# Performance work log

Hardware: AMD Instinct MI355X
Metric: run time of the kernel (lower is better)

The kernel has to match this reference:

```python
import jax, jax.numpy as jnp
import numpy as np

B, T, D, H = 2, 2048, 1024, 16
HD = D // H


def sinusoidal_rel_pe(seq_len, d_model, dtype=jnp.float32):
    # Relative positions T-1 .. 0 (reversed), standard sin/cos interleave.
    pos = jnp.arange(seq_len - 1, -1, -1, dtype=jnp.float32)[:, None]  # [T,1]
    div = jnp.exp(-jnp.log(jnp.float32(10000.0)) * jnp.arange(0, d_model, 2, dtype=jnp.float32) / d_model)
    pe = jnp.zeros((seq_len, d_model), dtype=jnp.float32)
    pe = pe.at[:, 0::2].set(jnp.sin(pos * div))
    pe = pe.at[:, 1::2].set(jnp.cos(pos * div))
    return pe.astype(dtype)


def relative_to_absolute(x):
    # x: [B,H,T,L] with L == T. Music-Transformer skew trick.
    b, h, t1, l = x.shape
    x = jnp.pad(x, ((0, 0), (0, 0), (0, 0), (1, 0)))          # pad left of last dim
    x = x.reshape(b, h, -1)
    x = jnp.pad(x, ((0, 0), (0, 0), (l - t1, 0)))
    x = x.reshape(b, h, 1 + t1, l)
    return x[:, :, 1:]


def setup_inputs() -> dict:
    key = jax.random.key(0)
    k1, k2, k3 = jax.random.split(key, 3)
    x = jax.random.normal(k1, (B, T, D), dtype=jnp.float32)
    # causal mask: True where attention is disallowed (j > i)
    mask = jnp.triu(jnp.ones((T, T), dtype=bool), k=1)[None, None]
    mask = jnp.broadcast_to(mask, (B, 1, T, T))
    Wqkv = jax.random.normal(k2, (D, 3 * D), dtype=jnp.float32) * 0.02
    Wout = jax.random.normal(k3, (D, D), dtype=jnp.float32) * 0.02
    bout = jnp.zeros((D,), dtype=jnp.float32)
    return {"x": x, "mask": mask, "Wqkv": Wqkv, "Wout": Wout, "bout": bout}


def reference(x, mask, Wqkv, Wout, bout):
    b, t, d = x.shape
    scale = jnp.sqrt(jnp.float32(HD)).astype(x.dtype)
    qkv = x @ Wqkv                                  # [B,T,3D]
    q, k, v = jnp.split(qkv, 3, axis=-1)
    E = sinusoidal_rel_pe(t, d, x.dtype)            # [T,D], constant rel bias
    q = q.reshape(b, t, H, HD).transpose(0, 2, 1, 3)   # [B,H,T,hd]
    k = k.reshape(b, t, H, HD).transpose(0, 2, 1, 3)
    v = v.reshape(b, t, H, HD).transpose(0, 2, 1, 3)
    Eh = E.reshape(t, H, HD).transpose(1, 0, 2)        # [H,T,hd]
    att_k = jnp.einsum('bhqd,bhkd->bhqk', q, k)
    att_e = relative_to_absolute(jnp.einsum('bhqd,hkd->bhqk', q, Eh))
    score = (att_k + att_e) / scale
    score = jnp.where(mask, -jnp.inf, score)
    score = jax.nn.softmax(score, axis=-1)          # dropout is identity (eval)
    ctx = jnp.einsum('bhqk,bhkd->bhqd', score, v)
    ctx = ctx.transpose(0, 2, 1, 3).reshape(b, t, d)
    out = ctx @ Wout + bout
    return (out, score)
```

## Files before the change

kernel.cpp:

```cpp
#include <hip/hip_runtime.h>

typedef __bf16 bf16x8 __attribute__((ext_vector_type(8)));
typedef float f32x4 __attribute__((ext_vector_type(4)));

#define B_ 2
#define T_ 2048
#define D_ 1024
#define H_ 16

__device__ __forceinline__ ushort f2bf(float f) {
  union { float f; unsigned u; } v; v.f = f;
  unsigned u = v.u;
  return (ushort)((u + 0x7FFFu + ((u >> 16) & 1u)) >> 16);
}

__device__ __forceinline__ void g2l16(const void* g, void* l) {
  __builtin_amdgcn_global_load_lds(
      (const __attribute__((address_space(1))) unsigned int*)g,
      (__attribute__((address_space(3))) unsigned int*)l, 16, 0, 0);
}

__global__ __launch_bounds__(256) void cvt_kernel(const float* __restrict__ in,
                                                  ushort* __restrict__ out) {
  int i = (blockIdx.x * 256 + threadIdx.x) * 4;
  float4 v = *(const float4*)(in + i);
  ushort4 o;
  o.x = f2bf(v.x); o.y = f2bf(v.y); o.z = f2bf(v.z); o.w = f2bf(v.w);
  *(ushort4*)(out + i) = o;
}

__global__ void transpose_cvt(const float* __restrict__ in, ushort* __restrict__ out,
                              int R, int C) {
  __shared__ float tile[32][33];
  int bx = blockIdx.x * 32, by = blockIdx.y * 32;
  int tx = threadIdx.x, ty = threadIdx.y;
  for (int i = 0; i < 32; i += 8)
    tile[ty + i][tx] = in[(size_t)(by + ty + i) * C + (bx + tx)];
  __syncthreads();
  for (int i = 0; i < 32; i += 8)
    out[(size_t)(bx + ty + i) * R + (by + tx)] = f2bf(tile[tx][ty + i]);
}

__global__ __launch_bounds__(256) void gemm_bf16(
    const ushort* __restrict__ A, const ushort* __restrict__ BT,
    float* __restrict__ C, const float* __restrict__ bias,
    int M, int N, int K) {
  __shared__ alignas(16) ushort As[2][4096];
  __shared__ alignas(16) ushort Bs[2][4096];
  int tid = threadIdx.x;
  int wave = tid >> 6, lane = tid & 63;
  int l16 = lane & 15, lhi = lane >> 4;
  int m0 = blockIdx.y * 128, n0 = blockIdx.x * 128;
  int wr = (wave >> 1) * 64, wc = (wave & 1) * 64;
  int srow = lane >> 2, sch = lane & 3;

  f32x4 acc[4][4] = {};

  auto stage = [&](int kk, int buf) {
    for (int i = 0; i < 2; ++i) {
      int rg = i * 4 + wave;
      const ushort* ga = A + (size_t)(m0 + rg * 16 + srow) * K + kk + sch * 8;
      const ushort* gb = BT + (size_t)(n0 + rg * 16 + srow) * K + kk + sch * 8;
      g2l16(ga, &As[buf][rg * 512]);
      g2l16(gb, &Bs[buf][rg * 512]);
    }
  };

  stage(0, 0);
  int buf = 0;
  for (int kk = 0; kk < K; kk += 32) {
    __syncthreads();
    if (kk + 32 < K) stage(kk + 32, buf ^ 1);
    const ushort* Asb = As[buf];
    const ushort* Bsb = Bs[buf];
    bf16x8 af[4], bfr[4];
    for (int f = 0; f < 4; ++f)
      af[f] = *(const bf16x8*)(Asb + (wr + f * 16 + l16) * 32 + lhi * 8);
    for (int f = 0; f < 4; ++f)
      bfr[f] = *(const bf16x8*)(Bsb + (wc + f * 16 + l16) * 32 + lhi * 8);
    for (int fm = 0; fm < 4; ++fm)
      for (int fn = 0; fn < 4; ++fn)
        acc[fm][fn] = __builtin_amdgcn_mfma_f32_16x16x32_bf16(af[fm], bfr[fn], acc[fm][fn], 0, 0, 0);
    buf ^= 1;
  }
  for (int fm = 0; fm < 4; ++fm)
    for (int fn = 0; fn < 4; ++fn)
      for (int r = 0; r < 4; ++r) {
        int row = m0 + wr + fm * 16 + lhi * 4 + r;
        int col = n0 + wc + fn * 16 + l16;
        float v = acc[fm][fn][r];
        if (bias) v += bias[col];
        C[(size_t)row * N + col] = v;
      }
}

__global__ __launch_bounds__(256) void augment_kernel(
    const float* __restrict__ qkv,
    ushort* __restrict__ Qaug, ushort* __restrict__ Kaug, ushort* __restrict__ Vb) {
  int row = blockIdx.x;
  int b = row >> 11;
  int t = row & 2047;
  int tid = threadIdx.x;
  const float* src = qkv + (size_t)row * 3072;
  for (int i = 0; i < 4; ++i) {
    int idx = tid + i * 256;
    int h = idx >> 6, d = idx & 63;
    size_t obase = ((size_t)(b * H_ + h) * T_ + t);
    float q = src[idx];
    float k = src[1024 + idx];
    float v = src[2048 + idx];
    Qaug[obase * 128 + d] = f2bf(q * 0.125f);
    Kaug[obase * 128 + d] = f2bf(k);
    Vb[obase * 64 + d] = f2bf(v);
  }
  for (int i = 0; i < 2; ++i) {
    int idx = tid + i * 256;
    int h = idx >> 5, mm = idx & 31;
    int gdim = h * 64 + 2 * mm;
    float w = __expf(-9.2103403719761836f * (float)gdim * (1.0f / 1024.0f));
    float ang = w * (float)t;
    float si, co;
    __sincosf(ang, &si, &co);
    float qs = src[h * 64 + 2 * mm], qc = src[h * 64 + 2 * mm + 1];
    size_t obase = ((size_t)(b * H_ + h) * T_ + t);
    Qaug[obase * 128 + 64 + 2 * mm]     = f2bf((qs * si + qc * co) * 0.125f);
    Qaug[obase * 128 + 64 + 2 * mm + 1] = f2bf((qc * si - qs * co) * 0.125f);
    Kaug[obase * 128 + 64 + 2 * mm]     = f2bf(co);
    Kaug[obase * 128 + 64 + 2 * mm + 1] = f2bf(si);
  }
}

__global__ __launch_bounds__(256) void transpose_v(const ushort* __restrict__ Vb,
                                                   ushort* __restrict__ Vt) {
  __shared__ ushort tile[64][72];
  int bh = blockIdx.y, t0 = blockIdx.x * 64;
  int tid = threadIdx.x;
  for (int i = 0; i < 2; ++i) {
    int e = tid + i * 256;
    int row = e >> 3, ch = e & 7;
    *(int4*)(&tile[row][ch * 8]) =
        *(const int4*)(Vb + ((size_t)bh * T_ + t0 + row) * 64 + ch * 8);
  }
  __syncthreads();
  for (int i = 0; i < 2; ++i) {
    int e = tid + i * 256;
    int d = e >> 3, ch = e & 7;
    union { int4 v; ushort u[8]; } pk;
    for (int u = 0; u < 8; ++u) pk.u[u] = tile[ch * 8 + u][d];
    *(int4*)(Vt + ((size_t)bh * 64 + d) * T_ + t0 + ch * 8) = pk.v;
  }
}

__global__ __launch_bounds__(256, 4) void denom_kernel(
    const ushort* __restrict__ Qaug,
    const ushort* __restrict__ Kaug,
    float* __restrict__ invlb) {
  int flat = blockIdx.y * 32 + blockIdx.x;
  int wg = (flat & 7) * 128 + (flat >> 3);
  int bh = wg >> 5;
  int qt = 31 - (wg & 31);
  int tid = threadIdx.x;
  int wave = tid >> 6, lane = tid & 63;
  int l16 = lane & 15, lhi = lane >> 4;
  int qb = wave * 16;
  int e7 = l16 & 7;

  __shared__ alignas(16) ushort Ks[2][8192];

  const ushort* Kbase = Kaug + (size_t)bh * T_ * 128;

  auto stageK = [&](int kt, int buf) {
    for (int i = 0; i < 4; ++i) {
      int rg = i * 4 + wave;
      int key = rg * 4 + (lane >> 4);
      const ushort* g = Kbase + ((size_t)(kt * 64 + key)) * 128 + (((lane & 15) ^ (key & 7)) << 3);
      g2l16(g, &Ks[buf][rg * 512]);
    }
  };

  bf16x8 qf[4];
  {
    const ushort* Qg = Qaug + ((size_t)bh * T_ + qt * 64 + qb + l16) * 128;
    for (int ks = 0; ks < 4; ++ks)
      qf[ks] = *(const bf16x8*)(Qg + ks * 32 + lhi * 8);
  }

  stageK(0, 0);
  asm volatile("s_waitcnt vmcnt(0)" ::: "memory");
  __builtin_amdgcn_s_barrier();
  float plsum[4] = {0.f, 0.f, 0.f, 0.f};
  for (int kt = 0; kt <= qt; ++kt) {
    int buf = kt & 1;
    if (kt < qt) stageK(kt + 1, buf ^ 1);
    __builtin_amdgcn_sched_barrier(0);
    const ushort* Kb = Ks[buf];
    f32x4 s[4] = {};
    for (int ks = 0; ks < 4; ++ks)
      for (int fn = 0; fn < 4; ++fn) {
        bf16x8 bfr = *(const bf16x8*)(Kb + (fn * 16 + l16) * 128 + ((((ks << 2) | lhi) ^ e7) << 3));
        s[fn] = __builtin_amdgcn_mfma_f32_16x16x32_bf16(qf[ks], bfr, s[fn], 0, 0, 0);
      }
    if (kt == qt) {
      for (int fn = 0; fn < 4; ++fn)
        for (int r = 0; r < 4; ++r)
          if (fn * 16 + l16 > qb + lhi * 4 + r) s[fn][r] = -1e30f;
    }
    for (int r = 0; r < 4; ++r)
      plsum[r] += __expf(s[0][r]) + __expf(s[1][r]) + __expf(s[2][r]) + __expf(s[3][r]);
    if (kt < qt) {
      asm volatile("s_waitcnt vmcnt(0)" ::: "memory");
      __builtin_amdgcn_s_barrier();
    }
  }
  for (int r = 0; r < 4; ++r) {
    float v = plsum[r];
    for (int dd = 1; dd < 16; dd <<= 1) v += __shfl_xor(v, dd);
    if (l16 == 0)
      invlb[(size_t)bh * T_ + qt * 64 + qb + lhi * 4 + r] = 1.f / v;
  }
}

__global__ __launch_bounds__(256) void attn2_kernel(
    const ushort* __restrict__ Qaug,
    const ushort* __restrict__ Kaug,
    const ushort* __restrict__ Vt,
    const float* __restrict__ invlb,
    float* __restrict__ score,
    ushort* __restrict__ ctxb) {
  int flat = blockIdx.y * 32 + blockIdx.x;
  int wg = (flat & 7) * 128 + (flat >> 3);
  int bh = wg >> 5;
  int qt = 31 - (wg & 31);
  int tid = threadIdx.x;
  int wave = tid >> 6, lane = tid & 63;
  int l16 = lane & 15, lhi = lane >> 4;
  int qb = wave * 16;
  int e7 = l16 & 7;

  __shared__ alignas(16) ushort Ks[2][8192];
  __shared__ alignas(16) ushort Vs[2][4096];
  __shared__ alignas(16) ushort Ps[4096];

  const ushort* Kbase = Kaug + (size_t)bh * T_ * 128;
  const ushort* Vbase = Vt + (size_t)bh * 64 * T_;

  auto stageK = [&](int kt, int buf) {
    for (int i = 0; i < 4; ++i) {
      int rg = i * 4 + wave;
      int key = rg * 4 + (lane >> 4);
      const ushort* g = Kbase + ((size_t)(kt * 64 + key)) * 128 + (((lane & 15) ^ (key & 7)) << 3);
      g2l16(g, &Ks[buf][rg * 512]);
    }
  };
  auto stageV = [&](int kt, int buf) {
    for (int i = 0; i < 2; ++i) {
      int rg = i * 4 + wave;
      int dim = rg * 8 + (lane >> 3);
      const ushort* g = Vbase + (size_t)dim * T_ + kt * 64 + (((lane & 7) ^ (dim & 7)) << 3);
      g2l16(g, &Vs[buf][rg * 512]);
    }
  };

  bf16x8 qf[4];
  {
    const ushort* Qg = Qaug + ((size_t)bh * T_ + qt * 64 + qb + l16) * 128;
    for (int ks = 0; ks < 4; ++ks)
      qf[ks] = *(const bf16x8*)(Qg + ks * 32 + lhi * 8);
  }
  float4 iv = *(const float4*)(invlb + (size_t)bh * T_ + qt * 64 + qb + lhi * 4);
  float invl[4] = {iv.x, iv.y, iv.z, iv.w};

  stageK(0, 0);
  stageV(0, 0);
  asm volatile("s_waitcnt vmcnt(0)" ::: "memory");
  __builtin_amdgcn_s_barrier();
  f32x4 cacc[4] = {};
  float* srow = score + ((size_t)bh * T_ + (size_t)qt * 64) * T_;

  for (int kt = 0; kt <= qt; ++kt) {
    int buf = kt & 1;
    if (kt < qt) { stageK(kt + 1, buf ^ 1); stageV(kt + 1, buf ^ 1); }
    __builtin_amdgcn_sched_barrier(0);
    const ushort* Kb = Ks[buf];
    f32x4 s[4] = {};
    for (int ks = 0; ks < 4; ++ks)
      for (int fn = 0; fn < 4; ++fn) {
        bf16x8 bfr = *(const bf16x8*)(Kb + (fn * 16 + l16) * 128 + ((((ks << 2) | lhi) ^ e7) << 3));
        s[fn] = __builtin_amdgcn_mfma_f32_16x16x32_bf16(qf[ks], bfr, s[fn], 0, 0, 0);
      }
    if (kt == qt) {
      for (int fn = 0; fn < 4; ++fn)
        for (int r = 0; r < 4; ++r)
          if (fn * 16 + l16 > qb + lhi * 4 + r) s[fn][r] = -1e30f;
    }
    for (int fn = 0; fn < 4; ++fn)
      for (int r = 0; r < 4; ++r) {
        int row_loc = qb + lhi * 4 + r;
        float p = __expf(s[fn][r]) * invl[r];
        srow[(size_t)row_loc * T_ + kt * 64 + fn * 16 + l16] = p;
        Ps[row_loc * 64 + (((fn * 2 + (l16 >> 3)) ^ (row_loc & 7)) << 3) + e7] = f2bf(p);
      }
    asm volatile("s_waitcnt lgkmcnt(0)" ::: "memory");
    __builtin_amdgcn_sched_barrier(0);
    const ushort* Vb2 = Vs[buf];
    for (int ks = 0; ks < 2; ++ks) {
      bf16x8 pa = *(const bf16x8*)(Ps + (qb + l16) * 64 + ((((ks << 2) | lhi) ^ e7) << 3));
      for (int fn = 0; fn < 4; ++fn) {
        bf16x8 vb = *(const bf16x8*)(Vb2 + (fn * 16 + l16) * 64 + ((((ks << 2) | lhi) ^ e7) << 3));
        cacc[fn] = __builtin_amdgcn_mfma_f32_16x16x32_bf16(pa, vb, cacc[fn], 0, 0, 0);
      }
    }
    if (kt < qt) {
      asm volatile("s_waitcnt vmcnt(16)" ::: "memory");
      __builtin_amdgcn_s_barrier();
    }
  }

  {
    int row = tid >> 2, c16 = (tid & 3) * 16;
    f32x4 z = {0.f, 0.f, 0.f, 0.f};
    for (int kt = qt + 1; kt < 32; ++kt) {
      f32x4* dst = (f32x4*)(srow + (size_t)row * T_ + kt * 64 + c16);
      for (int u = 0; u < 4; ++u) dst[u] = z;
    }
  }

  int b = bh >> 4, h = bh & 15;
  for (int fn = 0; fn < 4; ++fn)
    for (int r = 0; r < 4; ++r) {
      int t = qt * 64 + qb + lhi * 4 + r;
      int col = h * 64 + fn * 16 + l16;
      ctxb[((size_t)(b * T_ + t)) * 1024 + col] = f2bf(cacc[fn][r]);
    }
}

extern "C" void kernel_launch(void* const* d_in, const int* in_sizes, int n_in,
                              void* d_out, int out_size, void* d_ws, size_t ws_size,
                              hipStream_t stream) {
  const float* x    = (const float*)d_in[0];
  const float* Wqkv = (const float*)d_in[2];
  const float* Wout = (const float*)d_in[3];
  const float* bout = (const float*)d_in[4];

  char* ws = (char*)d_ws;
  ushort* xb    = (ushort*)(ws + 0);
  ushort* wqkvT = (ushort*)(ws + 8388608);
  ushort* woutT = (ushort*)(ws + 14680064);
  float*  qkv   = (float*) (ws + 16777216);
  ushort* Qaug  = (ushort*)(ws + 67108864);
  ushort* Kaug  = (ushort*)(ws + 83886080);
  ushort* Vb    = (ushort*)(ws + 100663296);
  ushort* ctxb  = (ushort*)(ws + 109051904);
  ushort* Vt    = (ushort*)(ws + 16777216);
  float*  invlb = (float*) (ws + 25165824);

  float* out   = (float*)d_out;
  float* score = out + (size_t)4194304;

  cvt_kernel<<<4096, 256, 0, stream>>>(x, xb);
  dim3 tb(32, 8);
  transpose_cvt<<<dim3(3072 / 32, 1024 / 32), tb, 0, stream>>>(Wqkv, wqkvT, 1024, 3072);
  transpose_cvt<<<dim3(1024 / 32, 1024 / 32), tb, 0, stream>>>(Wout, woutT, 1024, 1024);
  gemm_bf16<<<dim3(24, 32), 256, 0, stream>>>(xb, wqkvT, qkv, nullptr, 4096, 3072, 1024);
  augment_kernel<<<4096, 256, 0, stream>>>(qkv, Qaug, Kaug, Vb);
  transpose_v<<<dim3(32, 32), 256, 0, stream>>>(Vb, Vt);
  denom_kernel<<<dim3(32, 32), 256, 0, stream>>>(Qaug, Kaug, invlb);
  attn2_kernel<<<dim3(32, 32), 256, 0, stream>>>(Qaug, Kaug, Vt, invlb, score, ctxb);
  gemm_bf16<<<dim3(8, 32), 256, 0, stream>>>(ctxb, woutT, out, bout, 4096, 1024, 1024);
}
```

Before: 316.6 us.

## Switch attention and denominator kernels to 32x32x16 MFMA with 2x2 wave tiling

```diff
diff --git a/kernel.cpp b/kernel.cpp
--- a/kernel.cpp
+++ b/kernel.cpp
@@ -2,6 +2,7 @@
 
 typedef __bf16 bf16x8 __attribute__((ext_vector_type(8)));
 typedef float f32x4 __attribute__((ext_vector_type(4)));
+typedef float f32x16 __attribute__((ext_vector_type(16)));
 
 #define B_ 2
 #define T_ 2048
@@ -59,10 +60,8 @@
   auto stage = [&](int kk, int buf) {
     for (int i = 0; i < 2; ++i) {
       int rg = i * 4 + wave;
-      const ushort* ga = A + (size_t)(m0 + rg * 16 + srow) * K + kk + sch * 8;
-      const ushort* gb = BT + (size_t)(n0 + rg * 16 + srow) * K + kk + sch * 8;
-      g2l16(ga, &As[buf][rg * 512]);
-      g2l16(gb, &Bs[buf][rg * 512]);
+      g2l16(A + (size_t)(m0 + rg * 16 + srow) * K + kk + sch * 8, &As[buf][rg * 512]);
+      g2l16(BT + (size_t)(n0 + rg * 16 + srow) * K + kk + sch * 8, &Bs[buf][rg * 512]);
     }
   };
 
@@ -151,6 +150,10 @@
   }
 }
 
+__device__ __forceinline__ int rowf32(int reg, int hi) {
+  return (reg & 3) + 8 * (reg >> 2) + 4 * hi;
+}
+
 __global__ __launch_bounds__(256, 4) void denom_kernel(
     const ushort* __restrict__ Qaug,
     const ushort* __restrict__ Kaug,
@@ -161,11 +164,11 @@
   int qt = 31 - (wg & 31);
   int tid = threadIdx.x;
   int wave = tid >> 6, lane = tid & 63;
-  int l16 = lane & 15, lhi = lane >> 4;
-  int qb = wave * 16;
-  int e7 = l16 & 7;
+  int l31 = lane & 31, hi = lane >> 5;
+  int r = wave >> 1, d = wave & 1;
 
   __shared__ alignas(16) ushort Ks[2][8192];
+  __shared__ float sums[64];
 
   const ushort* Kbase = Kaug + (size_t)bh * T_ * 128;
 
@@ -173,51 +176,60 @@
     for (int i = 0; i < 4; ++i) {
       int rg = i * 4 + wave;
       int key = rg * 4 + (lane >> 4);
-      const ushort* g = Kbase + ((size_t)(kt * 64 + key)) * 128 + (((lane & 15) ^ (key & 7)) << 3);
+      const ushort* g = Kbase + ((size_t)(kt * 64 + key)) * 128 + (((lane & 15) ^ (key & 15)) << 3);
       g2l16(g, &Ks[buf][rg * 512]);
     }
   };
 
-  bf16x8 qf[4];
+  bf16x8 qf[8];
   {
-    const ushort* Qg = Qaug + ((size_t)bh * T_ + qt * 64 + qb + l16) * 128;
-    for (int ks = 0; ks < 4; ++ks)
-      qf[ks] = *(const bf16x8*)(Qg + ks * 32 + lhi * 8);
-  }
+    const ushort* Qg = Qaug + ((size_t)bh * T_ + qt * 64 + r * 32 + l31) * 128;
+    for (int ks = 0; ks < 8; ++ks)
+      qf[ks] = *(const bf16x8*)(Qg + ks * 16 + hi * 8);
+  }
+  int key = d * 32 + l31;
 
   stageK(0, 0);
   asm volatile("s_waitcnt vmcnt(0)" ::: "memory");
   __builtin_amdgcn_s_barrier();
-  float plsum[4] = {0.f, 0.f, 0.f, 0.f};
+  float plsum[16];
+  for (int i = 0; i < 16; ++i) plsum[i] = 0.f;
+
   for (int kt = 0; kt <= qt; ++kt) {
     int buf = kt & 1;
     if (kt < qt) stageK(kt + 1, buf ^ 1);
     __builtin_amdgcn_sched_barrier(0);
     const ushort* Kb = Ks[buf];
-    f32x4 s[4] = {};
-    for (int ks = 0; ks < 4; ++ks)
-      for (int fn = 0; fn < 4; ++fn) {
-        bf16x8 bfr = *(const bf16x8*)(Kb + (fn * 16 + l16) * 128 + ((((ks << 2) | lhi) ^ e7) << 3));
-        s[fn] = __builtin_amdgcn_mfma_f32_16x16x32_bf16(qf[ks], bfr, s[fn], 0, 0, 0);
-      }
+    f32x16 s = {};
+    for (int ks = 0; ks < 8; ++ks) {
+      int slot = (ks * 2 + hi) ^ (key & 15);
+      bf16x8 kf = *(const bf16x8*)(Kb + key * 128 + (slot << 3));
+      s = __builtin_amdgcn_mfma_f32_32x32x16_bf16(qf[ks], kf, s, 0, 0, 0);
+    }
     if (kt == qt) {
-      for (int fn = 0; fn < 4; ++fn)
-        for (int r = 0; r < 4; ++r)
-          if (fn * 16 + l16 > qb + lhi * 4 + r) s[fn][r] = -1e30f;
-    }
-    for (int r = 0; r < 4; ++r)
-      plsum[r] += __expf(s[0][r]) + __expf(s[1][r]) + __expf(s[2][r]) + __expf(s[3][r]);
+      for (int reg = 0; reg < 16; ++reg)
+        if (d * 32 + l31 > r * 32 + rowf32(reg, hi)) s[reg] = -1e30f;
+    }
+    for (int reg = 0; reg < 16; ++reg) plsum[reg] += __expf(s[reg]);
     if (kt < qt) {
       asm volatile("s_waitcnt vmcnt(0)" ::: "memory");
       __builtin_amdgcn_s_barrier();
     }
   }
-  for (int r = 0; r < 4; ++r) {
-    float v = plsum[r];
-    for (int dd = 1; dd < 16; dd <<= 1) v += __shfl_xor(v, dd);
-    if (l16 == 0)
-      invlb[(size_t)bh * T_ + qt * 64 + qb + lhi * 4 + r] = 1.f / v;
-  }
+  for (int reg = 0; reg < 16; ++reg) {
+    float v = plsum[reg];
+    for (int dd = 1; dd < 32; dd <<= 1) v += __shfl_xor(v, dd);
+    plsum[reg] = v;
+  }
+  if (d == 1 && l31 == 0)
+    for (int reg = 0; reg < 16; ++reg)
+      sums[r * 32 + rowf32(reg, hi)] = plsum[reg];
+  __syncthreads();
+  if (d == 0 && l31 == 0)
+    for (int reg = 0; reg < 16; ++reg) {
+      int row = r * 32 + rowf32(reg, hi);
+      invlb[(size_t)bh * T_ + qt * 64 + row] = 1.f / (plsum[reg] + sums[row]);
+    }
 }
 
 __global__ __launch_bounds__(256) void attn2_kernel(
@@ -233,9 +245,8 @@
   int qt = 31 - (wg & 31);
   int tid = threadIdx.x;
   int wave = tid >> 6, lane = tid & 63;
-  int l16 = lane & 15, lhi = lane >> 4;
-  int qb = wave * 16;
-  int e7 = l16 & 7;
+  int l31 = lane & 31, hi = lane >> 5;
+  int r = wave >> 1, d = wave & 1;
 
   __shared__ alignas(16) ushort Ks[2][8192];
   __shared__ alignas(16) ushort Vs[2][4096];
@@ -248,7 +259,7 @@
     for (int i = 0; i < 4; ++i) {
       int rg = i * 4 + wave;
       int key = rg * 4 + (lane >> 4);
-      const ushort* g = Kbase + ((size_t)(kt * 64 + key)) * 128 + (((lane & 15) ^ (key & 7)) << 3);
+      const ushort* g = Kbase + ((size_t)(kt * 64 + key)) * 128 + (((lane & 15) ^ (key & 15)) << 3);
       g2l16(g, &Ks[buf][rg * 512]);
     }
   };
@@ -261,20 +272,22 @@
     }
   };
 
-  bf16x8 qf[4];
+  bf16x8 qf[8];
   {
-    const ushort* Qg = Qaug + ((size_t)bh * T_ + qt * 64 + qb + l16) * 128;
-    for (int ks = 0; ks < 4; ++ks)
-      qf[ks] = *(const bf16x8*)(Qg + ks * 32 + lhi * 8);
-  }
-  float4 iv = *(const float4*)(invlb + (size_t)bh * T_ + qt * 64 + qb + lhi * 4);
-  float invl[4] = {iv.x, iv.y, iv.z, iv.w};
+    const ushort* Qg = Qaug + ((size_t)bh * T_ + qt * 64 + r * 32 + l31) * 128;
+    for (int ks = 0; ks < 8; ++ks)
+      qf[ks] = *(const bf16x8*)(Qg + ks * 16 + hi * 8);
+  }
+  int key = d * 32 + l31;
+  float4 iv[4];
+  for (int g = 0; g < 4; ++g)
+    iv[g] = *(const float4*)(invlb + (size_t)bh * T_ + qt * 64 + r * 32 + hi * 4 + g * 8);
 
   stageK(0, 0);
   stageV(0, 0);
   asm volatile("s_waitcnt vmcnt(0)" ::: "memory");
   __builtin_amdgcn_s_barrier();
-  f32x4 cacc[4] = {};
+  f32x16 cacc[2] = {};
   float* srow = score + ((size_t)bh * T_ + (size_t)qt * 64) * T_;
 
   for (int kt = 0; kt <= qt; ++kt) {
@@ -282,32 +295,33 @@
     if (kt < qt) { stageK(kt + 1, buf ^ 1); stageV(kt + 1, buf ^ 1); }
     __builtin_amdgcn_sched_barrier(0);
     const ushort* Kb = Ks[buf];
-    f32x4 s[4] = {};
-    for (int ks = 0; ks < 4; ++ks)
-      for (int fn = 0; fn < 4; ++fn) {
-        bf16x8 bfr = *(const bf16x8*)(Kb + (fn * 16 + l16) * 128 + ((((ks << 2) | lhi) ^ e7) << 3));
-        s[fn] = __builtin_amdgcn_mfma_f32_16x16x32_bf16(qf[ks], bfr, s[fn], 0, 0, 0);
-      }
+    f32x16 s = {};
+    for (int ks = 0; ks < 8; ++ks) {
+      int slot = (ks * 2 + hi) ^ (key & 15);
+      bf16x8 kf = *(const bf16x8*)(Kb + key * 128 + (slot << 3));
+      s = __builtin_amdgcn_mfma_f32_32x32x16_bf16(qf[ks], kf, s, 0, 0, 0);
+    }
     if (kt == qt) {
-      for (int fn = 0; fn < 4; ++fn)
-        for (int r = 0; r < 4; ++r)
-          if (fn * 16 + l16 > qb + lhi * 4 + r) s[fn][r] = -1e30f;
-    }
-    for (int fn = 0; fn < 4; ++fn)
-      for (int r = 0; r < 4; ++r) {
-        int row_loc = qb + lhi * 4 + r;
-        float p = __expf(s[fn][r]) * invl[r];
-        srow[(size_t)row_loc * T_ + kt * 64 + fn * 16 + l16] = p;
-        Ps[row_loc * 64 + (((fn * 2 + (l16 >> 3)) ^ (row_loc & 7)) << 3) + e7] = f2bf(p);
-      }
+      for (int reg = 0; reg < 16; ++reg)
+        if (d * 32 + l31 > r * 32 + rowf32(reg, hi)) s[reg] = -1e30f;
+    }
+    for (int reg = 0; reg < 16; ++reg) {
+      int row_loc = r * 32 + rowf32(reg, hi);
+      float p = __expf(s[reg]) * iv[reg >> 2][reg & 3];
+      srow[(size_t)row_loc * T_ + kt * 64 + key] = p;
+      Ps[row_loc * 64 + ((((key >> 3)) ^ (row_loc & 7)) << 3) + (key & 7)] = f2bf(p);
+    }
     asm volatile("s_waitcnt lgkmcnt(0)" ::: "memory");
     __builtin_amdgcn_sched_barrier(0);
     const ushort* Vb2 = Vs[buf];
-    for (int ks = 0; ks < 2; ++ks) {
-      bf16x8 pa = *(const bf16x8*)(Ps + (qb + l16) * 64 + ((((ks << 2) | lhi) ^ e7) << 3));
-      for (int fn = 0; fn < 4; ++fn) {
-        bf16x8 vb = *(const bf16x8*)(Vb2 + (fn * 16 + l16) * 64 + ((((ks << 2) | lhi) ^ e7) << 3));
-        cacc[fn] = __builtin_amdgcn_mfma_f32_16x16x32_bf16(pa, vb, cacc[fn], 0, 0, 0);
+    int rowA = r * 32 + l31;
+    for (int ks2 = 0; ks2 < 2; ++ks2) {
+      int chunkA = d * 4 + ks2 * 2 + hi;
+      bf16x8 pa = *(const bf16x8*)(Ps + rowA * 64 + ((chunkA ^ (rowA & 7)) << 3));
+      for (int b2 = 0; b2 < 2; ++b2) {
+        int dim = b2 * 32 + l31;
+        bf16x8 vb = *(const bf16x8*)(Vb2 + dim * 64 + ((chunkA ^ (dim & 7)) << 3));
+        cacc[b2] = __builtin_amdgcn_mfma_f32_32x32x16_bf16(pa, vb, cacc[b2], 0, 0, 0);
       }
     }
     if (kt < qt) {
@@ -325,13 +339,24 @@
     }
   }
 
-  int b = bh >> 4, h = bh & 15;
-  for (int fn = 0; fn < 4; ++fn)
-    for (int r = 0; r < 4; ++r) {
-      int t = qt * 64 + qb + lhi * 4 + r;
-      int col = h * 64 + fn * 16 + l16;
-      ctxb[((size_t)(b * T_ + t)) * 1024 + col] = f2bf(cacc[fn][r]);
-    }
+  __builtin_amdgcn_s_barrier();
+  float* xch = (float*)Ks;
+  if (d == 1) {
+    for (int b2 = 0; b2 < 2; ++b2)
+      for (int reg = 0; reg < 16; ++reg)
+        xch[(r * 32 + rowf32(reg, hi)) * 64 + b2 * 32 + l31] = cacc[b2][reg];
+  }
+  __syncthreads();
+  if (d == 0) {
+    int b = bh >> 4, h = bh & 15;
+    for (int b2 = 0; b2 < 2; ++b2)
+      for (int reg = 0; reg < 16; ++reg) {
+        int row_loc = r * 32 + rowf32(reg, hi);
+        float v = cacc[b2][reg] + xch[row_loc * 64 + b2 * 32 + l31];
+        int t = qt * 64 + row_loc;
+        ctxb[((size_t)(b * T_ + t)) * 1024 + h * 64 + b2 * 32 + l31] = f2bf(v);
+      }
+  }
 }
 
 extern "C" void kernel_launch(void* const* d_in, const int* in_sizes, int n_in,
```

Measured after the change: 315.2 us. Within noise of the previous version (-0.5%).
